# Kernel optimization log

Hardware: AMD Instinct MI355X
Metric: run time of the kernel (lower is better)

The kernel has to match this reference:

```python
import jax, jax.numpy as jnp
import numpy as np

KC = 32      # cluster_num
KS = 3       # kernel_size
AREA = KS * KS
ITERS = 10   # KMeans Lloyd iterations (fixed, deterministic init)


def _unfold3(x):
    # torch nn.Unfold(kernel_size=3, padding=1): feature dim ordered cin-major, area-minor
    b, c, h, w = x.shape
    xp = jnp.pad(x, ((0, 0), (0, 0), (1, 1), (1, 1)))
    cols = jnp.stack([xp[:, :, i:i + h, j:j + w] for i in range(KS) for j in range(KS)], axis=2)  # [b,c,area,h,w]
    return cols.reshape(b, c * AREA, h * w).transpose(0, 2, 1)  # [b, hw, c*area]


def _kmeans_assign(feat):
    # Lloyd's KMeans on [s, d] features; deterministic strided init; returns [s] int assignments
    s, d = feat.shape
    c0 = feat[jnp.arange(KC) * (s // KC)]
    f2 = (feat * feat).sum(-1, keepdims=True)
    def dists(c):
        return f2 - 2.0 * feat @ c.T + (c * c).sum(-1)[None, :]
    def step(c, _):
        idx = jnp.argmin(dists(c), axis=1)
        cnt = jax.ops.segment_sum(jnp.ones((s,), feat.dtype), idx, KC)
        sm = jax.ops.segment_sum(feat, idx, KC)
        c_new = jnp.where(cnt[:, None] > 0, sm / jnp.maximum(cnt, 1.0)[:, None], c)
        return c_new, None
    c, _ = jax.lax.scan(step, c0, None, length=ITERS)
    return jnp.argmin(dists(c), axis=1)


def _seg_mean(p, idx):
    # per-cluster mean of patches -> patch-space centroids [K, f]
    s = p.shape[0]
    cnt = jax.ops.segment_sum(jnp.ones((s,), p.dtype), idx, KC)
    return jax.ops.segment_sum(p, idx, KC) / jnp.maximum(cnt, 1.0)[:, None]


def _mlp2(x, W1, b1, W2, b2):
    return jax.nn.relu(jax.nn.relu(x @ W1 + b1) @ W2 + b2)


def setup_inputs():
    key = jax.random.key(0)
    ks = jax.random.split(key, 16)
    cin, cout, m = 32, 32, 16
    f = cin * AREA
    g = lambda k, shp, sc: jax.random.normal(k, shp, dtype=jnp.float32) * sc
    return {
        "x": g(ks[0], (4, cin, 64, 64), 1.0),
        "Wh1": g(ks[1], (f, m), (2.0 / f) ** 0.5), "bh1": jnp.zeros((m,), jnp.float32),
        "Wh2": g(ks[2], (m, m), (2.0 / m) ** 0.5), "bh2": jnp.zeros((m,), jnp.float32),
        "Wa": g(ks[3], (m, AREA), (2.0 / m) ** 0.5), "ba": jnp.zeros((AREA,), jnp.float32),
        "Wc": g(ks[4], (m, cin), (2.0 / m) ** 0.5), "bc": jnp.zeros((cin,), jnp.float32),
        "Wo": g(ks[5], (m, cout), (2.0 / m) ** 0.5), "bo": jnp.zeros((cout,), jnp.float32),
        "kernels": g(ks[6], (cin, AREA, cout), (2.0 / (cin * AREA)) ** 0.5),
        "Wb1": g(ks[7], (f, m), (2.0 / f) ** 0.5), "bb1": jnp.zeros((m,), jnp.float32),
        "Wb2": g(ks[8], (m, m), (2.0 / m) ** 0.5), "bb2": jnp.zeros((m,), jnp.float32),
        "Wb3": g(ks[9], (m, cout), (2.0 / m) ** 0.5), "bb3": jnp.zeros((cout,), jnp.float32),
    }


def reference(x, Wh1, bh1, Wh2, bh2, Wa, ba, Wc, bc, Wo, bo, kernels, Wb1, bb1, Wb2, bb2, Wb3, bb3):
    b, cin, h, w = x.shape
    s = h * w
    cout = kernels.shape[-1]
    patches = _unfold3(x)                                        # [b, s, cin*area]
    feat = patches.reshape(b, s, cin, AREA).mean(-1)             # cluster_source='channel'
    idx = jax.vmap(_kmeans_assign)(jax.lax.stop_gradient(feat))  # [b, s] cluster assignments
    centroids = jax.vmap(_seg_mean)(patches, idx)                # [b, K, cin*area]
    # low_rank kernel generator: rank-1 modulation along cin/area/cout of shared base kernel
    kf = _mlp2(centroids, Wh1, bh1, Wh2, bh2)                    # [b, K, m]
    w_cin = jax.nn.sigmoid(kf @ Wc + bc)                         # [b, K, cin]
    w_area = jax.nn.sigmoid(kf @ Wa + ba)                        # [b, K, area]
    w_cout = jax.nn.sigmoid(kf @ Wo + bo)                        # [b, K, cout]
    kern = (w_cin[:, :, :, None, None] * w_area[:, :, None, :, None]
            * w_cout[:, :, None, None, :] * kernels[None, None])  # [b, K, cin, area, cout]
    kern = kern.reshape(b, KC, cin * AREA, cout)
    bias = _mlp2(centroids, Wb1, bb1, Wb2, bb2) @ Wb3 + bb3      # [b, K, cout] (bias='cluster')
    # gather per-pixel kernel/bias by cluster id, grouped matmul, scatter back (dense-gather form)
    bi = jnp.arange(b)[:, None]
    Wpix = kern[bi, idx]                                         # [b, s, f, cout]
    out = jnp.einsum('bsf,bsfo->bso', patches, Wpix) + bias[bi, idx]
    return out.reshape(b, h, w, cout).transpose(0, 3, 1, 2), idx
```

## Files before the change

kernel.cpp:

```cpp
#include <hip/hip_runtime.h>
#include <stdint.h>

typedef unsigned long long u64;

#define Bn 4
#define CINn 32
#define Hn 64
#define Wn 64
#define Sn 4096
#define KCn 32
#define Mn 16
#define COUTn 32
#define AREAn 9
#define Fn 288
#define NITER 10
#define FXSCALE 4294967296.0
#define NBLK_B 32
#define LDK 292

#define AT_LD_U32(p)    __hip_atomic_load((p),  __ATOMIC_RELAXED, __HIP_MEMORY_SCOPE_AGENT)
#define AT_LD_U64(p)    __hip_atomic_load((p),  __ATOMIC_RELAXED, __HIP_MEMORY_SCOPE_AGENT)
#define AT_ST_U32(p,v)  __hip_atomic_store((p), (v), __ATOMIC_RELAXED, __HIP_MEMORY_SCOPE_AGENT)
#define AT_ST_U64(p,v)  __hip_atomic_store((p), (v), __ATOMIC_RELAXED, __HIP_MEMORY_SCOPE_AGENT)

static __device__ __forceinline__ float relu_(float v){ return v > 0.f ? v : 0.f; }
static __device__ __forceinline__ float sigmoid_(float v){ return 1.f / (1.f + expf(-v)); }

static __device__ __forceinline__ void batch_barrier(unsigned* bar){
    __syncthreads();
    if (threadIdx.x == 0){
        asm volatile("s_waitcnt vmcnt(0)" ::: "memory");
        unsigned* cnt = bar;
        unsigned* gen = bar + 32;
        unsigned g = __hip_atomic_load(gen, __ATOMIC_RELAXED, __HIP_MEMORY_SCOPE_AGENT);
        unsigned a = __hip_atomic_fetch_add(cnt, 1u, __ATOMIC_RELAXED, __HIP_MEMORY_SCOPE_AGENT);
        if (a == (unsigned)(NBLK_B - 1)){
            __hip_atomic_store(cnt, 0u, __ATOMIC_RELAXED, __HIP_MEMORY_SCOPE_AGENT);
            __hip_atomic_fetch_add(gen, 1u, __ATOMIC_RELAXED, __HIP_MEMORY_SCOPE_AGENT);
        } else {
            while (__hip_atomic_load(gen, __ATOMIC_RELAXED, __HIP_MEMORY_SCOPE_AGENT) == g)
                __builtin_amdgcn_s_sleep(4);
        }
    }
    __syncthreads();
}

__global__ __launch_bounds__(256) void k_init(const float* __restrict__ x,
                                              float* __restrict__ feat,
                                              u64* __restrict__ gsum,
                                              unsigned* __restrict__ gcnt,
                                              unsigned* __restrict__ bar){
    int g = blockIdx.x * 256 + threadIdx.x;
    if (g < 3 * Bn * KCn * CINn) gsum[g] = 0ull;
    if (g < 3 * Bn * KCn)        gcnt[g] = 0u;
    if (g < 4 * 64)              bar[g]  = 0u;
    int p = g & (Sn - 1);
    int c = (g >> 12) & (CINn - 1);
    int b = g >> 17;
    int y = p >> 6, xx = p & 63;
    const float* xc = x + ((size_t)(b * CINn + c) << 12);
    float s = 0.f;
    #pragma unroll
    for (int i = 0; i < 3; ++i){
        int yy = y + i - 1;
        if (yy < 0 || yy >= Hn) continue;
        #pragma unroll
        for (int j = 0; j < 3; ++j){
            int xj = xx + j - 1;
            if (xj < 0 || xj >= Wn) continue;
            s += xc[(yy << 6) + xj];
        }
    }
    feat[g] = s * (1.f / 9.f);
}

struct AssignSh {
    u64   fxL[128][32];
    u64   lsum[KCn][CINn];
    float cent[KCn][CINn];
    float c2[KCn];
    float bestd[256];
    int   bestk[256];
    int   bi128[128];
    unsigned lcnt[KCn];
    unsigned cntPrev[KCn];
    int   rankF[128];
    unsigned totK[KCn];
    unsigned goffK[KCn + 1];
    unsigned baseBT[KCn];
};
struct SmkSh {
    float psum[KCn][AREAn][8];
    float centL[Fn];
    int   pl[256];
    float part1[16][16], part2[16][16];
    float hL[2][Mn];
    float kfL[2][Mn];
};
union ShU { AssignSh a; SmkSh m; };

__global__ __launch_bounds__(256) void k_main(const float* __restrict__ x,
        const float* __restrict__ feat,
        u64* __restrict__ gsum, unsigned* __restrict__ gcnt,
        unsigned* __restrict__ blkcnt,
        int* __restrict__ idx, float* __restrict__ idxf,
        int* __restrict__ sorted,
        const float* __restrict__ Wh1, const float* __restrict__ bh1,
        const float* __restrict__ Wh2, const float* __restrict__ bh2,
        const float* __restrict__ Wa,  const float* __restrict__ ba,
        const float* __restrict__ Wc,  const float* __restrict__ bc,
        const float* __restrict__ Wo,  const float* __restrict__ bo,
        const float* __restrict__ Wb1, const float* __restrict__ bb1,
        const float* __restrict__ Wb2, const float* __restrict__ bb2,
        const float* __restrict__ Wb3, const float* __restrict__ bb3,
        float* __restrict__ wcin, float* __restrict__ warea,
        float* __restrict__ wcout, float* __restrict__ biasb,
        unsigned* __restrict__ bars){
    __shared__ ShU sh;
    const int tid  = threadIdx.x;
    const int b    = blockIdx.x >> 5;
    const int tnum = blockIdx.x & 31;
    unsigned* bar  = bars + b * 64;

    const int pxi  = tid & 127;
    const int half = tid >> 7;
    const int p    = tnum * 128 + pxi;

    float fv[CINn];
    #pragma unroll
    for (int c = 0; c < CINn; ++c) fv[c] = feat[(b * CINn + c) * Sn + p];
    float f2 = 0.f;
    #pragma unroll
    for (int c = 0; c < CINn; ++c) f2 = fmaf(fv[c], fv[c], f2);
    if (tid < 128){
        #pragma unroll
        for (int c = 0; c < CINn; ++c)
            sh.a.fxL[tid][c] = (u64)llrint((double)fv[c] * FXSCALE);
    }

    for (int iter = 0; iter <= NITER; ++iter){
        const int prev = (iter + 2) % 3;
        const int cur  = iter % 3;
        const int nxt  = (iter + 1) % 3;

        if (iter > 0 && tid < KCn)
            sh.a.cntPrev[tid] = AT_LD_U32(&gcnt[(prev * Bn + b) * KCn + tid]);
        __syncthreads();

        for (int e = tid; e < KCn * CINn; e += 256){
            int k = e >> 5, c = e & 31;
            if (iter == 0){
                sh.a.cent[k][c] = feat[(b * CINn + c) * Sn + k * (Sn / KCn)];
            } else {
                unsigned cn = sh.a.cntPrev[k];
                if (cn > 0){
                    u64 sv = AT_LD_U64(&gsum[((prev * Bn + b) * KCn + k) * CINn + c]);
                    sh.a.cent[k][c] = (float)((double)(long long)sv / ((double)cn * FXSCALE));
                }
            }
            sh.a.lsum[k][c] = 0ull;
            if (tnum == 0)
                AT_ST_U64(&gsum[((nxt * Bn + b) * KCn + k) * CINn + c], 0ull);
        }
        if (tnum == 0 && tid < KCn)
            AT_ST_U32(&gcnt[(nxt * Bn + b) * KCn + tid], 0u);
        __syncthreads();

        if (tid < 32){
            float s = 0.f;
            #pragma unroll
            for (int c = 0; c < CINn; ++c) s = fmaf(sh.a.cent[tid][c], sh.a.cent[tid][c], s);
            sh.a.c2[tid] = s;
        } else if (tid < 64){
            sh.a.lcnt[tid - 32] = 0u;
        }
        __syncthreads();

        float best = 3.402823466e38f;
        int   bk   = half << 4;
        #pragma unroll 4
        for (int k = 0; k < 16; ++k){
            const int kk = (half << 4) + k;
            const float4* cr4 = reinterpret_cast<const float4*>(sh.a.cent[kk]);
            float dot = 0.f;
            #pragma unroll
            for (int cq = 0; cq < 8; ++cq){
                float4 cv = cr4[cq];
                dot = fmaf(fv[cq * 4 + 0], cv.x, dot);
                dot = fmaf(fv[cq * 4 + 1], cv.y, dot);
                dot = fmaf(fv[cq * 4 + 2], cv.z, dot);
                dot = fmaf(fv[cq * 4 + 3], cv.w, dot);
            }
            float d = f2 - 2.f * dot + sh.a.c2[kk];
            if (d < best){ best = d; bk = kk; }
        }
        sh.a.bestd[tid] = best;
        sh.a.bestk[tid] = bk;
        __syncthreads();

        if (tid < 128){
            float d0 = sh.a.bestd[tid], d1 = sh.a.bestd[tid + 128];
            int   k0 = sh.a.bestk[tid], k1 = sh.a.bestk[tid + 128];
            int bi = (d1 < d0) ? k1 : k0;
            sh.a.bi128[tid] = bi;
            if (iter < NITER) atomicAdd(&sh.a.lcnt[bi], 1u);
        }
        __syncthreads();

        if (iter < NITER){
            {
                const int myk = sh.a.bi128[pxi];
                const int c0  = half << 4;
                #pragma unroll
                for (int c = 0; c < 16; ++c)
                    atomicAdd(&sh.a.lsum[myk][c0 + c], sh.a.fxL[pxi][c0 + c]);
            }
            __syncthreads();
            for (int e = tid; e < KCn * CINn; e += 256){
                int k = e >> 5, c = e & 31;
                u64 v = sh.a.lsum[k][c];
                if (v) atomicAdd(&gsum[((cur * Bn + b) * KCn + k) * CINn + c], v);
            }
            if (tid < KCn){
                unsigned v = sh.a.lcnt[tid];
                if (v) atomicAdd(&gcnt[(cur * Bn + b) * KCn + tid], v);
            }
        } else {
            if (tid < 128){
                int bi = sh.a.bi128[tid];
                idx [b * Sn + p] = bi;
                idxf[b * Sn + p] = (float)bi;
            }
            __syncthreads();
            if (tid < KCn){
                int r = 0;
                for (int q = 0; q < 128; ++q)
                    if (sh.a.bi128[q] == tid) sh.a.rankF[q] = r++;
                AT_ST_U32(&blkcnt[(b * KCn + tid) * NBLK_B + tnum], (unsigned)r);
            }
        }
        batch_barrier(bar);
    }

    if (tid < KCn){
        unsigned run = 0, mybase = 0;
        #pragma unroll 4
        for (int t2 = 0; t2 < NBLK_B; ++t2){
            unsigned v = AT_LD_U32(&blkcnt[(b * KCn + tid) * NBLK_B + t2]);
            if (t2 == tnum) mybase = run;
            run += v;
        }
        sh.a.totK[tid]   = run;
        sh.a.baseBT[tid] = mybase;
    }
    __syncthreads();
    if (tid == 0){
        unsigned acc = 0;
        #pragma unroll
        for (int k = 0; k < KCn; ++k){ sh.a.goffK[k] = acc; acc += sh.a.totK[k]; }
        sh.a.goffK[KCn] = acc;
    }
    __syncthreads();
    if (tid < 128){
        int k = sh.a.bi128[tid];
        unsigned pos = sh.a.goffK[k] + sh.a.baseBT[k] + (unsigned)sh.a.rankF[tid];
        AT_ST_U32((unsigned*)&sorted[b * Sn + pos], (unsigned)(tnum * 128 + tid));
    }
    const int kk    = tnum;
    const int off0r = (int)sh.a.goffK[kk];
    const int nmy   = (int)sh.a.totK[kk];
    batch_barrier(bar);

    {
        const int cA = tid >> 3;
        const int s  = tid & 7;
        const float* xc = x + ((size_t)(b * CINn + cA) << 12);
        float acc[9];
        #pragma unroll
        for (int a = 0; a < 9; ++a) acc[a] = 0.f;

        for (int base = 0; base < nmy; base += 256){
            int m = min(256, nmy - base);
            __syncthreads();
            if (tid < m)
                sh.m.pl[tid] = (int)AT_LD_U32((unsigned*)&sorted[b * Sn + off0r + base + tid]);
            __syncthreads();
            #pragma unroll 2
            for (int i = s; i < m; i += 8){
                int pp = sh.m.pl[i];
                int py = pp >> 6, px2 = pp & 63;
                #pragma unroll
                for (int a = 0; a < 9; ++a){
                    int y1 = py + a / 3 - 1, x1 = px2 + (a % 3) - 1;
                    float v = (y1 >= 0 && y1 < Hn && x1 >= 0 && x1 < Wn)
                              ? xc[(y1 << 6) + x1] : 0.f;
                    acc[a] += v;
                }
            }
        }
        __syncthreads();
        #pragma unroll
        for (int a = 0; a < 9; ++a) sh.m.psum[cA][a][s] = acc[a];
        __syncthreads();
        float invn = 1.f / (float)max(nmy, 1);
        for (int f = tid; f < Fn; f += 256){
            int c = f / 9, a = f - c * 9;
            float sm = 0.f;
            #pragma unroll
            for (int s2 = 0; s2 < 8; ++s2) sm += sh.m.psum[c][a][s2];
            sh.m.centL[f] = sm * invn;
        }
    }
    __syncthreads();

    {
        int j = tid & 15, rep = tid >> 4;
        float p1 = 0.f, p2 = 0.f;
        int fbeg = rep * 18;
        for (int ff = fbeg; ff < fbeg + 18; ++ff){
            float cv = sh.m.centL[ff];
            p1 = fmaf(cv, Wh1[ff * Mn + j], p1);
            p2 = fmaf(cv, Wb1[ff * Mn + j], p2);
        }
        sh.m.part1[rep][j] = p1;
        sh.m.part2[rep][j] = p2;
    }
    __syncthreads();
    if (tid < 32){
        int br = tid >> 4, j = tid & 15;
        float s = br ? bb1[j] : bh1[j];
        for (int r = 0; r < 16; ++r) s += br ? sh.m.part2[r][j] : sh.m.part1[r][j];
        sh.m.hL[br][j] = relu_(s);
    }
    __syncthreads();
    if (tid < 32){
        int br = tid >> 4, j = tid & 15;
        const float* W2 = br ? Wb2 : Wh2;
        float s = br ? bb2[j] : bh2[j];
        #pragma unroll
        for (int i = 0; i < Mn; ++i) s = fmaf(sh.m.hL[br][i], W2[i * Mn + j], s);
        sh.m.kfL[br][j] = relu_(s);
    }
    __syncthreads();
    if (tid < 32){
        int o = tid;
        float s1 = bc[o], s2 = bo[o], s3 = bb3[o];
        #pragma unroll
        for (int i = 0; i < Mn; ++i){
            float kv = sh.m.kfL[0][i];
            s1 = fmaf(kv, Wc[i * COUTn + o], s1);
            s2 = fmaf(kv, Wo[i * COUTn + o], s2);
            s3 = fmaf(sh.m.kfL[1][i], Wb3[i * COUTn + o], s3);
        }
        wcin [(b * KCn + kk) * CINn  + o] = sigmoid_(s1);
        wcout[(b * KCn + kk) * COUTn + o] = sigmoid_(s2);
        biasb[(b * KCn + kk) * COUTn + o] = s3;
    } else if (tid < 41){
        int a2 = tid - 32;
        float s = ba[a2];
        #pragma unroll
        for (int i = 0; i < Mn; ++i) s = fmaf(sh.m.kfL[0][i], Wa[i * AREAn + a2], s);
        warea[(b * KCn + kk) * AREAn + a2] = sigmoid_(s);
    }
}

__global__ __launch_bounds__(256) void k_out(const float* __restrict__ x,
                                             const int* __restrict__ sorted,
                                             const int* __restrict__ idx,
                                             const float* __restrict__ wcin,
                                             const float* __restrict__ warea,
                                             const float* __restrict__ wcout,
                                             const float* __restrict__ biasb,
                                             const float* __restrict__ kern0,
                                             float* __restrict__ out){
    int b    = blockIdx.x >> 7;
    int tile = blockIdx.x & 127;
    int tid  = threadIdx.x;

    __shared__ float kernT[KCn * LDK];
    __shared__ float patchL[32 * LDK];
    __shared__ int   pix[32];
    __shared__ int   kid[32];
    __shared__ float wcl[CINn], wal[AREAn], wol[COUTn], biasL[COUTn];

    if (tid < 32){
        int pp = sorted[b * Sn + tile * 32 + tid];
        pix[tid] = pp;
        kid[tid] = idx[b * Sn + pp];
    }
    int fA = tid;       int cA = fA / 9, aA = fA - cA * 9;
    int dyA = aA / 3 - 1, dxA = aA % 3 - 1;
    int fB = 256 + tid; int cB = fB / 9, aB = fB - cB * 9;
    int dyB = aB / 3 - 1, dxB = aB % 3 - 1;
    __syncthreads();

    #pragma unroll 4
    for (int px = 0; px < 32; ++px){
        int pp = pix[px];
        int py = pp >> 6, pxx = pp & 63;
        int y1 = py + dyA, x1 = pxx + dxA;
        patchL[px * LDK + tid] = (y1 >= 0 && y1 < Hn && x1 >= 0 && x1 < Wn)
            ? x[((size_t)(b * CINn + cA) << 12) + (y1 << 6) + x1] : 0.f;
        if (tid < 32){
            int y2 = py + dyB, x2 = pxx + dxB;
            patchL[px * LDK + 256 + tid] = (y2 >= 0 && y2 < Hn && x2 >= 0 && x2 < Wn)
                ? x[((size_t)(b * CINn + cB) << 12) + (y2 << 6) + x2] : 0.f;
        }
    }

    int o2 = tid & 15, p2 = tid >> 4;
    int oA = o2 * 2, oB = o2 * 2 + 1;
    int pxA = p2 * 2, pxB = p2 * 2 + 1;

    int i0 = 0;
    while (i0 < 32){
        __syncthreads();
        int kcur = kid[i0];
        int i1 = i0 + 1;
        while (i1 < 32 && kid[i1] == kcur) ++i1;

        if (tid < 32)       wcl[tid]        = wcin [(b * KCn + kcur) * CINn  + tid];
        else if (tid < 64)  wol[tid - 32]   = wcout[(b * KCn + kcur) * COUTn + tid - 32];
        else if (tid < 73)  wal[tid - 64]   = warea[(b * KCn + kcur) * AREAn + tid - 64];
        else if (tid >= 96 && tid < 128) biasL[tid - 96] = biasb[(b * KCn + kcur) * COUTn + tid - 96];
        __syncthreads();

        {
            int o  = tid >> 3;
            int q  = tid & 7;
            int f0 = q * 36;
            int cc = q * 4, aa = 0;
            float wo_ = wol[o];
            float* kr = kernT + o * LDK + f0;
            #pragma unroll 4
            for (int i2 = 0; i2 < 36; ++i2){
                kr[i2] = wcl[cc] * wal[aa] * wo_ * kern0[(f0 + i2) * COUTn + o];
                if (++aa == 9){ aa = 0; ++cc; }
            }
        }
        __syncthreads();

        bool actA = (pxA >= i0 && pxA < i1);
        bool actB = (pxB >= i0 && pxB < i1);
        if (actA || actB){
            const float* krA = kernT + oA * LDK;
            const float* krB = kernT + oB * LDK;
            const float* prA = patchL + pxA * LDK;
            const float* prB = patchL + pxB * LDK;
            float s00 = 0.f, s01 = 0.f, s10 = 0.f, s11 = 0.f;
            if (actA && actB){
                #pragma unroll 4
                for (int fq = 0; fq < Fn; fq += 4){
                    float4 k0 = *reinterpret_cast<const float4*>(krA + fq);
                    float4 k1 = *reinterpret_cast<const float4*>(krB + fq);
                    float4 pa = *reinterpret_cast<const float4*>(prA + fq);
                    float4 pb = *reinterpret_cast<const float4*>(prB + fq);
                    s00 = fmaf(pa.x,k0.x,s00); s00 = fmaf(pa.y,k0.y,s00); s00 = fmaf(pa.z,k0.z,s00); s00 = fmaf(pa.w,k0.w,s00);
                    s01 = fmaf(pa.x,k1.x,s01); s01 = fmaf(pa.y,k1.y,s01); s01 = fmaf(pa.z,k1.z,s01); s01 = fmaf(pa.w,k1.w,s01);
                    s10 = fmaf(pb.x,k0.x,s10); s10 = fmaf(pb.y,k0.y,s10); s10 = fmaf(pb.z,k0.z,s10); s10 = fmaf(pb.w,k0.w,s10);
                    s11 = fmaf(pb.x,k1.x,s11); s11 = fmaf(pb.y,k1.y,s11); s11 = fmaf(pb.z,k1.z,s11); s11 = fmaf(pb.w,k1.w,s11);
                }
            } else {
                const float* pr = actA ? prA : prB;
                #pragma unroll 4
                for (int fq = 0; fq < Fn; fq += 4){
                    float4 k0 = *reinterpret_cast<const float4*>(krA + fq);
                    float4 k1 = *reinterpret_cast<const float4*>(krB + fq);
                    float4 pa = *reinterpret_cast<const float4*>(pr + fq);
                    s00 = fmaf(pa.x,k0.x,s00); s00 = fmaf(pa.y,k0.y,s00); s00 = fmaf(pa.z,k0.z,s00); s00 = fmaf(pa.w,k0.w,s00);
                    s01 = fmaf(pa.x,k1.x,s01); s01 = fmaf(pa.y,k1.y,s01); s01 = fmaf(pa.z,k1.z,s01); s01 = fmaf(pa.w,k1.w,s01);
                }
                if (actB){ s10 = s00; s11 = s01; s00 = 0.f; s01 = 0.f; }
            }
            if (actA){
                int pp = pix[pxA];
                out[((size_t)(b * COUTn + oA) << 12) + pp] = biasL[oA] + s00;
                out[((size_t)(b * COUTn + oB) << 12) + pp] = biasL[oB] + s01;
            }
            if (actB){
                int pp = pix[pxB];
                out[((size_t)(b * COUTn + oA) << 12) + pp] = biasL[oA] + s10;
                out[((size_t)(b * COUTn + oB) << 12) + pp] = biasL[oB] + s11;
            }
        }
        i0 = i1;
    }
}

extern "C" void kernel_launch(void* const* d_in, const int* in_sizes, int n_in,
                              void* d_out, int out_size, void* d_ws, size_t ws_size,
                              hipStream_t stream){
    const float* x    = (const float*)d_in[0];
    const float* Wh1  = (const float*)d_in[1];
    const float* bh1  = (const float*)d_in[2];
    const float* Wh2  = (const float*)d_in[3];
    const float* bh2  = (const float*)d_in[4];
    const float* Wa   = (const float*)d_in[5];
    const float* ba   = (const float*)d_in[6];
    const float* Wc   = (const float*)d_in[7];
    const float* bc   = (const float*)d_in[8];
    const float* Wo   = (const float*)d_in[9];
    const float* bo   = (const float*)d_in[10];
    const float* kern0= (const float*)d_in[11];
    const float* Wb1  = (const float*)d_in[12];
    const float* bb1  = (const float*)d_in[13];
    const float* Wb2  = (const float*)d_in[14];
    const float* bb2  = (const float*)d_in[15];
    const float* Wb3  = (const float*)d_in[16];
    const float* bb3  = (const float*)d_in[17];

    char* ws = (char*)d_ws;
    float*    feat   = (float*)(ws + 0);
    u64*      gsum   = (u64*)  (ws + 2097152);
    unsigned* gcnt   = (unsigned*)(ws + 2195456);
    unsigned* blkcnt = (unsigned*)(ws + 2196992);
    int*      idx    = (int*)  (ws + 2213376);
    int*      sorted = (int*)  (ws + 2278912);
    float*    wcin   = (float*)(ws + 2344448);
    float*    warea  = (float*)(ws + 2360832);
    float*    wcout  = (float*)(ws + 2365440);
    float*    biasb  = (float*)(ws + 2381824);
    unsigned* bars   = (unsigned*)(ws + 2398208);

    float* outp = (float*)d_out;
    float* idxf = outp + (size_t)Bn * COUTn * Sn;

    k_init<<<(Bn * CINn * Sn) / 256, 256, 0, stream>>>(x, feat, gsum, gcnt, bars);
    k_main<<<Bn * NBLK_B, 256, 0, stream>>>(x, feat, gsum, gcnt, blkcnt, idx, idxf,
                                            sorted,
                                            Wh1, bh1, Wh2, bh2, Wa, ba, Wc, bc, Wo, bo,
                                            Wb1, bb1, Wb2, bb2, Wb3, bb3,
                                            wcin, warea, wcout, biasb, bars);
    k_out<<<Bn * 128, 256, 0, stream>>>(x, sorted, idx, wcin, warea, wcout, biasb,
                                        kern0, outp);
}
```

Baseline: 225.5 us.

## Restructure k-means reduction, patch centroid accumulation and output chunking per cluster

Halves the blocks per batch to 16 with one pixel per thread. Each block now writes its own partial sums and counts, and every block reduces over all block partials, so global atomics and the triple-buffered zeroing go away. Patch-space centroids are accumulated per block in shared memory and atomically added to a global buffer, so each cluster no longer gathers its own pixels after the barrier. The output kernel launches one block per 32-pixel chunk of a single cluster using a precomputed chunk map, which removes the in-block loop over mixed clusters. The risks are fewer blocks for the k-means phase and heavier shared-memory float atomics.

```diff
diff --git a/kernel.cpp b/kernel.cpp
--- a/kernel.cpp
+++ b/kernel.cpp
@@ -15,11 +15,14 @@
 #define Fn 288
 #define NITER 10
 #define FXSCALE 4294967296.0
-#define NBLK_B 32
+#define NBLK_B 16
+#define PXB 256
+#define CMAX 160
 #define LDK 292
 
 #define AT_LD_U32(p)    __hip_atomic_load((p),  __ATOMIC_RELAXED, __HIP_MEMORY_SCOPE_AGENT)
 #define AT_LD_U64(p)    __hip_atomic_load((p),  __ATOMIC_RELAXED, __HIP_MEMORY_SCOPE_AGENT)
+#define AT_LD_F32(p)    __hip_atomic_load((p),  __ATOMIC_RELAXED, __HIP_MEMORY_SCOPE_AGENT)
 #define AT_ST_U32(p,v)  __hip_atomic_store((p), (v), __ATOMIC_RELAXED, __HIP_MEMORY_SCOPE_AGENT)
 #define AT_ST_U64(p,v)  __hip_atomic_store((p), (v), __ATOMIC_RELAXED, __HIP_MEMORY_SCOPE_AGENT)
 
@@ -39,7 +42,7 @@
             __hip_atomic_fetch_add(gen, 1u, __ATOMIC_RELAXED, __HIP_MEMORY_SCOPE_AGENT);
         } else {
             while (__hip_atomic_load(gen, __ATOMIC_RELAXED, __HIP_MEMORY_SCOPE_AGENT) == g)
-                __builtin_amdgcn_s_sleep(4);
+                __builtin_amdgcn_s_sleep(2);
         }
     }
     __syncthreads();
@@ -47,13 +50,11 @@
 
 __global__ __launch_bounds__(256) void k_init(const float* __restrict__ x,
                                               float* __restrict__ feat,
-                                              u64* __restrict__ gsum,
-                                              unsigned* __restrict__ gcnt,
+                                              float* __restrict__ gpsum,
                                               unsigned* __restrict__ bar){
     int g = blockIdx.x * 256 + threadIdx.x;
-    if (g < 3 * Bn * KCn * CINn) gsum[g] = 0ull;
-    if (g < 3 * Bn * KCn)        gcnt[g] = 0u;
-    if (g < 4 * 64)              bar[g]  = 0u;
+    if (g < Bn * KCn * Fn) gpsum[g] = 0.f;
+    if (g < Bn * 64)       bar[g]   = 0u;
     int p = g & (Sn - 1);
     int c = (g >> 12) & (CINn - 1);
     int b = g >> 17;
@@ -75,24 +76,17 @@
 }
 
 struct AssignSh {
-    u64   fxL[128][32];
-    u64   lsum[KCn][CINn];
     float cent[KCn][CINn];
     float c2[KCn];
-    float bestd[256];
-    int   bestk[256];
-    int   bi128[128];
+    u64   lsum[KCn][CINn];
     unsigned lcnt[KCn];
-    unsigned cntPrev[KCn];
-    int   rankF[128];
-    unsigned totK[KCn];
-    unsigned goffK[KCn + 1];
+    unsigned cntTot[KCn];
+    int   rankF[PXB];
     unsigned baseBT[KCn];
 };
 struct SmkSh {
-    float psum[KCn][AREAn][8];
+    float psum[KCn][Fn];
     float centL[Fn];
-    int   pl[256];
     float part1[16][16], part2[16][16];
     float hL[2][Mn];
     float kfL[2][Mn];
@@ -101,10 +95,10 @@
 
 __global__ __launch_bounds__(256) void k_main(const float* __restrict__ x,
         const float* __restrict__ feat,
-        u64* __restrict__ gsum, unsigned* __restrict__ gcnt,
+        u64* __restrict__ bsum, unsigned* __restrict__ bcnt,
         unsigned* __restrict__ blkcnt,
         int* __restrict__ idx, float* __restrict__ idxf,
-        int* __restrict__ sorted,
+        int* __restrict__ sorted, int4* __restrict__ chunk_map,
         const float* __restrict__ Wh1, const float* __restrict__ bh1,
         const float* __restrict__ Wh2, const float* __restrict__ bh2,
         const float* __restrict__ Wa,  const float* __restrict__ ba,
@@ -115,16 +109,18 @@
         const float* __restrict__ Wb3, const float* __restrict__ bb3,
         float* __restrict__ wcin, float* __restrict__ warea,
         float* __restrict__ wcout, float* __restrict__ biasb,
+        float* __restrict__ gpsum,
         unsigned* __restrict__ bars){
+    __shared__ int bi256[PXB];
+    __shared__ unsigned totK[KCn];
+    __shared__ unsigned goffK[KCn + 1];
     __shared__ ShU sh;
+
     const int tid  = threadIdx.x;
-    const int b    = blockIdx.x >> 5;
-    const int tnum = blockIdx.x & 31;
+    const int b    = blockIdx.x >> 4;
+    const int tnum = blockIdx.x & 15;
     unsigned* bar  = bars + b * 64;
-
-    const int pxi  = tid & 127;
-    const int half = tid >> 7;
-    const int p    = tnum * 128 + pxi;
+    const int p    = tnum * PXB + tid;
 
     float fv[CINn];
     #pragma unroll
@@ -132,56 +128,49 @@
     float f2 = 0.f;
     #pragma unroll
     for (int c = 0; c < CINn; ++c) f2 = fmaf(fv[c], fv[c], f2);
-    if (tid < 128){
-        #pragma unroll
-        for (int c = 0; c < CINn; ++c)
-            sh.a.fxL[tid][c] = (u64)llrint((double)fv[c] * FXSCALE);
-    }
 
     for (int iter = 0; iter <= NITER; ++iter){
-        const int prev = (iter + 2) % 3;
-        const int cur  = iter % 3;
-        const int nxt  = (iter + 1) % 3;
-
-        if (iter > 0 && tid < KCn)
-            sh.a.cntPrev[tid] = AT_LD_U32(&gcnt[(prev * Bn + b) * KCn + tid]);
-        __syncthreads();
-
-        for (int e = tid; e < KCn * CINn; e += 256){
-            int k = e >> 5, c = e & 31;
-            if (iter == 0){
+        if (iter == 0){
+            for (int e = tid; e < KCn * CINn; e += 256){
+                int k = e >> 5, c = e & 31;
                 sh.a.cent[k][c] = feat[(b * CINn + c) * Sn + k * (Sn / KCn)];
-            } else {
-                unsigned cn = sh.a.cntPrev[k];
-                if (cn > 0){
-                    u64 sv = AT_LD_U64(&gsum[((prev * Bn + b) * KCn + k) * CINn + c]);
-                    sh.a.cent[k][c] = (float)((double)(long long)sv / ((double)cn * FXSCALE));
-                }
-            }
-            sh.a.lsum[k][c] = 0ull;
-            if (tnum == 0)
-                AT_ST_U64(&gsum[((nxt * Bn + b) * KCn + k) * CINn + c], 0ull);
-        }
-        if (tnum == 0 && tid < KCn)
-            AT_ST_U32(&gcnt[(nxt * Bn + b) * KCn + tid], 0u);
-        __syncthreads();
-
-        if (tid < 32){
+            }
+        } else {
+            if (tid < KCn){
+                unsigned s = 0;
+                #pragma unroll 4
+                for (int blk = 0; blk < NBLK_B; ++blk)
+                    s += AT_LD_U32(&bcnt[(b * NBLK_B + blk) * KCn + tid]);
+                sh.a.cntTot[tid] = s;
+            }
+            __syncthreads();
+            for (int e = tid; e < KCn * CINn; e += 256){
+                int k = e >> 5, c = e & 31;
+                u64 s = 0;
+                #pragma unroll 4
+                for (int blk = 0; blk < NBLK_B; ++blk)
+                    s += AT_LD_U64(&bsum[((size_t)(b * NBLK_B + blk) * KCn + k) * CINn + c]);
+                unsigned cn = sh.a.cntTot[k];
+                if (cn > 0)
+                    sh.a.cent[k][c] = (float)((double)(long long)s / ((double)cn * FXSCALE));
+            }
+        }
+        __syncthreads();
+        if (tid < KCn){
             float s = 0.f;
             #pragma unroll
             for (int c = 0; c < CINn; ++c) s = fmaf(sh.a.cent[tid][c], sh.a.cent[tid][c], s);
             sh.a.c2[tid] = s;
-        } else if (tid < 64){
-            sh.a.lcnt[tid - 32] = 0u;
-        }
-        __syncthreads();
-
-        float best = 3.402823466e38f;
-        int   bk   = half << 4;
+            sh.a.lcnt[tid] = 0u;
+        }
+        for (int e = tid; e < KCn * CINn; e += 256)
+            ((u64*)sh.a.lsum)[e] = 0ull;
+        __syncthreads();
+
+        float best = 3.402823466e38f; int bk = 0;
         #pragma unroll 4
-        for (int k = 0; k < 16; ++k){
-            const int kk = (half << 4) + k;
-            const float4* cr4 = reinterpret_cast<const float4*>(sh.a.cent[kk]);
+        for (int k = 0; k < KCn; ++k){
+            const float4* cr4 = reinterpret_cast<const float4*>(sh.a.cent[k]);
             float dot = 0.f;
             #pragma unroll
             for (int cq = 0; cq < 8; ++cq){
@@ -191,51 +180,34 @@
                 dot = fmaf(fv[cq * 4 + 2], cv.z, dot);
                 dot = fmaf(fv[cq * 4 + 3], cv.w, dot);
             }
-            float d = f2 - 2.f * dot + sh.a.c2[kk];
-            if (d < best){ best = d; bk = kk; }
-        }
-        sh.a.bestd[tid] = best;
-        sh.a.bestk[tid] = bk;
-        __syncthreads();
-
-        if (tid < 128){
-            float d0 = sh.a.bestd[tid], d1 = sh.a.bestd[tid + 128];
-            int   k0 = sh.a.bestk[tid], k1 = sh.a.bestk[tid + 128];
-            int bi = (d1 < d0) ? k1 : k0;
-            sh.a.bi128[tid] = bi;
-            if (iter < NITER) atomicAdd(&sh.a.lcnt[bi], 1u);
-        }
-        __syncthreads();
+            float d = f2 - 2.f * dot + sh.a.c2[k];
+            if (d < best){ best = d; bk = k; }
+        }
+        bi256[tid] = bk;
 
         if (iter < NITER){
-            {
-                const int myk = sh.a.bi128[pxi];
-                const int c0  = half << 4;
-                #pragma unroll
-                for (int c = 0; c < 16; ++c)
-                    atomicAdd(&sh.a.lsum[myk][c0 + c], sh.a.fxL[pxi][c0 + c]);
+            atomicAdd(&sh.a.lcnt[bk], 1u);
+            #pragma unroll
+            for (int c = 0; c < CINn; ++c){
+                u64 q = (u64)llrint((double)fv[c] * FXSCALE);
+                atomicAdd(&sh.a.lsum[bk][c], q);
             }
             __syncthreads();
             for (int e = tid; e < KCn * CINn; e += 256){
                 int k = e >> 5, c = e & 31;
-                u64 v = sh.a.lsum[k][c];
-                if (v) atomicAdd(&gsum[((cur * Bn + b) * KCn + k) * CINn + c], v);
-            }
-            if (tid < KCn){
-                unsigned v = sh.a.lcnt[tid];
-                if (v) atomicAdd(&gcnt[(cur * Bn + b) * KCn + tid], v);
-            }
+                AT_ST_U64(&bsum[((size_t)(b * NBLK_B + tnum) * KCn + k) * CINn + c],
+                          sh.a.lsum[k][c]);
+            }
+            if (tid < KCn)
+                AT_ST_U32(&bcnt[(b * NBLK_B + tnum) * KCn + tid], sh.a.lcnt[tid]);
         } else {
-            if (tid < 128){
-                int bi = sh.a.bi128[tid];
-                idx [b * Sn + p] = bi;
-                idxf[b * Sn + p] = (float)bi;
-            }
+            idx [b * Sn + p] = bk;
+            idxf[b * Sn + p] = (float)bk;
             __syncthreads();
             if (tid < KCn){
                 int r = 0;
-                for (int q = 0; q < 128; ++q)
-                    if (sh.a.bi128[q] == tid) sh.a.rankF[q] = r++;
+                for (int q = 0; q < PXB; ++q)
+                    if (bi256[q] == tid) sh.a.rankF[q] = r++;
                 AT_ST_U32(&blkcnt[(b * KCn + tid) * NBLK_B + tnum], (unsigned)r);
             }
         }
@@ -245,245 +217,228 @@
     if (tid < KCn){
         unsigned run = 0, mybase = 0;
         #pragma unroll 4
-        for (int t2 = 0; t2 < NBLK_B; ++t2){
-            unsigned v = AT_LD_U32(&blkcnt[(b * KCn + tid) * NBLK_B + t2]);
-            if (t2 == tnum) mybase = run;
+        for (int blk = 0; blk < NBLK_B; ++blk){
+            unsigned v = AT_LD_U32(&blkcnt[(b * KCn + tid) * NBLK_B + blk]);
+            if (blk == tnum) mybase = run;
             run += v;
         }
-        sh.a.totK[tid]   = run;
+        totK[tid] = run;
         sh.a.baseBT[tid] = mybase;
     }
     __syncthreads();
     if (tid == 0){
         unsigned acc = 0;
         #pragma unroll
-        for (int k = 0; k < KCn; ++k){ sh.a.goffK[k] = acc; acc += sh.a.totK[k]; }
-        sh.a.goffK[KCn] = acc;
-    }
-    __syncthreads();
-    if (tid < 128){
-        int k = sh.a.bi128[tid];
-        unsigned pos = sh.a.goffK[k] + sh.a.baseBT[k] + (unsigned)sh.a.rankF[tid];
-        AT_ST_U32((unsigned*)&sorted[b * Sn + pos], (unsigned)(tnum * 128 + tid));
-    }
-    const int kk    = tnum;
-    const int off0r = (int)sh.a.goffK[kk];
-    const int nmy   = (int)sh.a.totK[kk];
+        for (int k = 0; k < KCn; ++k){ goffK[k] = acc; acc += totK[k]; }
+        goffK[KCn] = acc;
+    }
+    __syncthreads();
+    {
+        int k = bi256[tid];
+        unsigned pos = goffK[k] + sh.a.baseBT[k] + (unsigned)sh.a.rankF[tid];
+        sorted[b * Sn + pos] = p;
+    }
+    if (tnum == 0 && tid == 0){
+        int j = 0;
+        for (int k = 0; k < KCn; ++k){
+            int n = (int)totK[k];
+            for (int cb = 0; cb < n; cb += 32){
+                chunk_map[b * CMAX + j] = make_int4(k, (int)goffK[k] + cb, min(32, n - cb), 0);
+                ++j;
+            }
+        }
+        for (; j < CMAX; ++j) chunk_map[b * CMAX + j] = make_int4(-1, 0, 0, 0);
+    }
+    __syncthreads();
+
+    for (int e = tid; e < KCn * Fn; e += 256) ((float*)sh.m.psum)[e] = 0.f;
+    __syncthreads();
+    {
+        const int cc   = tid >> 3;
+        const int slot = tid & 7;
+        const float* xc = x + ((size_t)(b * CINn + cc) << 12);
+        for (int i = slot; i < PXB; i += 8){
+            int k  = bi256[i];
+            int pp = tnum * PXB + i;
+            int py = pp >> 6, px2 = pp & 63;
+            float* ps = &sh.m.psum[k][cc * 9];
+            #pragma unroll
+            for (int a = 0; a < 9; ++a){
+                int y1 = py + a / 3 - 1, x1 = px2 + (a % 3) - 1;
+                float v = (y1 >= 0 && y1 < Hn && x1 >= 0 && x1 < Wn)
+                          ? xc[(y1 << 6) + x1] : 0.f;
+                atomicAdd(&ps[a], v);
+            }
+        }
+    }
+    __syncthreads();
+    for (int e = tid; e < KCn * Fn; e += 256){
+        float v = ((float*)sh.m.psum)[e];
+        if (v != 0.f) atomicAdd(&gpsum[(size_t)b * KCn * Fn + e], v);
+    }
     batch_barrier(bar);
 
-    {
-        const int cA = tid >> 3;
-        const int s  = tid & 7;
-        const float* xc = x + ((size_t)(b * CINn + cA) << 12);
-        float acc[9];
-        #pragma unroll
-        for (int a = 0; a < 9; ++a) acc[a] = 0.f;
-
-        for (int base = 0; base < nmy; base += 256){
-            int m = min(256, nmy - base);
-            __syncthreads();
-            if (tid < m)
-                sh.m.pl[tid] = (int)AT_LD_U32((unsigned*)&sorted[b * Sn + off0r + base + tid]);
-            __syncthreads();
-            #pragma unroll 2
-            for (int i = s; i < m; i += 8){
-                int pp = sh.m.pl[i];
-                int py = pp >> 6, px2 = pp & 63;
-                #pragma unroll
-                for (int a = 0; a < 9; ++a){
-                    int y1 = py + a / 3 - 1, x1 = px2 + (a % 3) - 1;
-                    float v = (y1 >= 0 && y1 < Hn && x1 >= 0 && x1 < Wn)
-                              ? xc[(y1 << 6) + x1] : 0.f;
-                    acc[a] += v;
-                }
-            }
-        }
-        __syncthreads();
-        #pragma unroll
-        for (int a = 0; a < 9; ++a) sh.m.psum[cA][a][s] = acc[a];
-        __syncthreads();
-        float invn = 1.f / (float)max(nmy, 1);
-        for (int f = tid; f < Fn; f += 256){
-            int c = f / 9, a = f - c * 9;
-            float sm = 0.f;
-            #pragma unroll
-            for (int s2 = 0; s2 < 8; ++s2) sm += sh.m.psum[c][a][s2];
-            sh.m.centL[f] = sm * invn;
-        }
-    }
-    __syncthreads();
-
-    {
-        int j = tid & 15, rep = tid >> 4;
-        float p1 = 0.f, p2 = 0.f;
-        int fbeg = rep * 18;
-        for (int ff = fbeg; ff < fbeg + 18; ++ff){
-            float cv = sh.m.centL[ff];
-            p1 = fmaf(cv, Wh1[ff * Mn + j], p1);
-            p2 = fmaf(cv, Wb1[ff * Mn + j], p2);
-        }
-        sh.m.part1[rep][j] = p1;
-        sh.m.part2[rep][j] = p2;
-    }
-    __syncthreads();
-    if (tid < 32){
-        int br = tid >> 4, j = tid & 15;
-        float s = br ? bb1[j] : bh1[j];
-        for (int r = 0; r < 16; ++r) s += br ? sh.m.part2[r][j] : sh.m.part1[r][j];
-        sh.m.hL[br][j] = relu_(s);
-    }
-    __syncthreads();
-    if (tid < 32){
-        int br = tid >> 4, j = tid & 15;
-        const float* W2 = br ? Wb2 : Wh2;
-        float s = br ? bb2[j] : bh2[j];
-        #pragma unroll
-        for (int i = 0; i < Mn; ++i) s = fmaf(sh.m.hL[br][i], W2[i * Mn + j], s);
-        sh.m.kfL[br][j] = relu_(s);
-    }
-    __syncthreads();
-    if (tid < 32){
-        int o = tid;
-        float s1 = bc[o], s2 = bo[o], s3 = bb3[o];
-        #pragma unroll
-        for (int i = 0; i < Mn; ++i){
-            float kv = sh.m.kfL[0][i];
-            s1 = fmaf(kv, Wc[i * COUTn + o], s1);
-            s2 = fmaf(kv, Wo[i * COUTn + o], s2);
-            s3 = fmaf(sh.m.kfL[1][i], Wb3[i * COUTn + o], s3);
-        }
-        wcin [(b * KCn + kk) * CINn  + o] = sigmoid_(s1);
-        wcout[(b * KCn + kk) * COUTn + o] = sigmoid_(s2);
-        biasb[(b * KCn + kk) * COUTn + o] = s3;
-    } else if (tid < 41){
-        int a2 = tid - 32;
-        float s = ba[a2];
-        #pragma unroll
-        for (int i = 0; i < Mn; ++i) s = fmaf(sh.m.kfL[0][i], Wa[i * AREAn + a2], s);
-        warea[(b * KCn + kk) * AREAn + a2] = sigmoid_(s);
+    for (int kq = 0; kq < 2; ++kq){
+        const int kk = tnum + kq * 16;
+        const float invn = 1.f / (float)max(totK[kk], 1u);
+        __syncthreads();
+        for (int f = tid; f < Fn; f += 256)
+            sh.m.centL[f] = AT_LD_F32(&gpsum[((size_t)b * KCn + kk) * Fn + f]) * invn;
+        __syncthreads();
+        {
+            int j = tid & 15, rep = tid >> 4;
+            float p1 = 0.f, p2 = 0.f;
+            int fbeg = rep * 18;
+            for (int ff = fbeg; ff < fbeg + 18; ++ff){
+                float cv = sh.m.centL[ff];
+                p1 = fmaf(cv, Wh1[ff * Mn + j], p1);
+                p2 = fmaf(cv, Wb1[ff * Mn + j], p2);
+            }
+            sh.m.part1[rep][j] = p1;
+            sh.m.part2[rep][j] = p2;
+        }
+        __syncthreads();
+        if (tid < 32){
+            int br = tid >> 4, j = tid & 15;
+            float s = br ? bb1[j] : bh1[j];
+            for (int r = 0; r < 16; ++r) s += br ? sh.m.part2[r][j] : sh.m.part1[r][j];
+            sh.m.hL[br][j] = relu_(s);
+        }
+        __syncthreads();
+        if (tid < 32){
+            int br = tid >> 4, j = tid & 15;
+            const float* W2 = br ? Wb2 : Wh2;
+            float s = br ? bb2[j] : bh2[j];
+            #pragma unroll
+            for (int i = 0; i < Mn; ++i) s = fmaf(sh.m.hL[br][i], W2[i * Mn + j], s);
+            sh.m.kfL[br][j] = relu_(s);
+        }
+        __syncthreads();
+        if (tid < 32){
+            int o = tid;
+            float s1 = bc[o], s2 = bo[o], s3 = bb3[o];
+            #pragma unroll
+            for (int i = 0; i < Mn; ++i){
+                float kv = sh.m.kfL[0][i];
+                s1 = fmaf(kv, Wc[i * COUTn + o], s1);
+                s2 = fmaf(kv, Wo[i * COUTn + o], s2);
+                s3 = fmaf(sh.m.kfL[1][i], Wb3[i * COUTn + o], s3);
+            }
+            wcin [(b * KCn + kk) * CINn  + o] = sigmoid_(s1);
+            wcout[(b * KCn + kk) * COUTn + o] = sigmoid_(s2);
+            biasb[(b * KCn + kk) * COUTn + o] = s3;
+        } else if (tid < 41){
+            int a2 = tid - 32;
+            float s = ba[a2];
+            #pragma unroll
+            for (int i = 0; i < Mn; ++i) s = fmaf(sh.m.kfL[0][i], Wa[i * AREAn + a2], s);
+            warea[(b * KCn + kk) * AREAn + a2] = sigmoid_(s);
+        }
     }
 }
 
 __global__ __launch_bounds__(256) void k_out(const float* __restrict__ x,
                                              const int* __restrict__ sorted,
-                                             const int* __restrict__ idx,
+                                             const int4* __restrict__ chunk_map,
                                              const float* __restrict__ wcin,
                                              const float* __restrict__ warea,
                                              const float* __restrict__ wcout,
                                              const float* __restrict__ biasb,
                                              const float* __restrict__ kern0,
                                              float* __restrict__ out){
-    int b    = blockIdx.x >> 7;
-    int tile = blockIdx.x & 127;
-    int tid  = threadIdx.x;
-
-    __shared__ float kernT[KCn * LDK];
+    const int b   = blockIdx.x / CMAX;
+    const int j   = blockIdx.x - b * CMAX;
+    const int tid = threadIdx.x;
+
+    int4 cm = chunk_map[b * CMAX + j];
+    const int kcur = cm.x;
+    if (kcur < 0) return;
+    const int base = cm.y;
+    const int cnt  = cm.z;
+
+    __shared__ float kernT[COUTn * LDK];
     __shared__ float patchL[32 * LDK];
     __shared__ int   pix[32];
-    __shared__ int   kid[32];
     __shared__ float wcl[CINn], wal[AREAn], wol[COUTn], biasL[COUTn];
 
     if (tid < 32){
-        int pp = sorted[b * Sn + tile * 32 + tid];
-        pix[tid] = pp;
-        kid[tid] = idx[b * Sn + pp];
-    }
-    int fA = tid;       int cA = fA / 9, aA = fA - cA * 9;
-    int dyA = aA / 3 - 1, dxA = aA % 3 - 1;
-    int fB = 256 + tid; int cB = fB / 9, aB = fB - cB * 9;
-    int dyB = aB / 3 - 1, dxB = aB % 3 - 1;
-    __syncthreads();
+        pix[tid] = (tid < cnt) ? sorted[b * Sn + base + tid] : -1;
+    } else if (tid < 64)  wcl[tid - 32]    = wcin [(b * KCn + kcur) * CINn  + tid - 32];
+    else if (tid < 96)    wol[tid - 64]    = wcout[(b * KCn + kcur) * COUTn + tid - 64];
+    else if (tid < 105)   wal[tid - 96]    = warea[(b * KCn + kcur) * AREAn + tid - 96];
+    else if (tid >= 128 && tid < 160) biasL[tid - 128] = biasb[(b * KCn + kcur) * COUTn + tid - 128];
+
+    const int fA = tid;       const int cA = fA / 9, aA = fA - cA * 9;
+    const int dyA = aA / 3 - 1, dxA = aA % 3 - 1;
+    const int fB = 256 + tid; const int cB = fB / 9, aB = fB - cB * 9;
+    const int dyB = aB / 3 - 1, dxB = aB % 3 - 1;
+    __syncthreads();
+
+    {
+        int o  = tid >> 3;
+        int q  = tid & 7;
+        int f0 = q * 36;
+        int cc = q * 4, aa = 0;
+        float wo_ = wol[o];
+        float* kr = kernT + o * LDK + f0;
+        #pragma unroll 4
+        for (int i2 = 0; i2 < 36; ++i2){
+            kr[i2] = wcl[cc] * wal[aa] * wo_ * kern0[(f0 + i2) * COUTn + o];
+            if (++aa == 9){ aa = 0; ++cc; }
+        }
+    }
 
     #pragma unroll 4
     for (int px = 0; px < 32; ++px){
         int pp = pix[px];
-        int py = pp >> 6, pxx = pp & 63;
-        int y1 = py + dyA, x1 = pxx + dxA;
-        patchL[px * LDK + tid] = (y1 >= 0 && y1 < Hn && x1 >= 0 && x1 < Wn)
-            ? x[((size_t)(b * CINn + cA) << 12) + (y1 << 6) + x1] : 0.f;
-        if (tid < 32){
-            int y2 = py + dyB, x2 = pxx + dxB;
-            patchL[px * LDK + 256 + tid] = (y2 >= 0 && y2 < Hn && x2 >= 0 && x2 < Wn)
-                ? x[((size_t)(b * CINn + cB) << 12) + (y2 << 6) + x2] : 0.f;
-        }
-    }
-
-    int o2 = tid & 15, p2 = tid >> 4;
-    int oA = o2 * 2, oB = o2 * 2 + 1;
-    int pxA = p2 * 2, pxB = p2 * 2 + 1;
-
-    int i0 = 0;
-    while (i0 < 32){
-        __syncthreads();
-        int kcur = kid[i0];
-        int i1 = i0 + 1;
-        while (i1 < 32 && kid[i1] == kcur) ++i1;
-
-        if (tid < 32)       wcl[tid]        = wcin [(b * KCn + kcur) * CINn  + tid];
-        else if (tid < 64)  wol[tid - 32]   = wcout[(b * KCn + kcur) * COUTn + tid - 32];
-        else if (tid < 73)  wal[tid - 64]   = warea[(b * KCn + kcur) * AREAn + tid - 64];
-        else if (tid >= 96 && tid < 128) biasL[tid - 96] = biasb[(b * KCn + kcur) * COUTn + tid - 96];
-        __syncthreads();
-
-        {
-            int o  = tid >> 3;
-            int q  = tid & 7;
-            int f0 = q * 36;
-            int cc = q * 4, aa = 0;
-            float wo_ = wol[o];
-            float* kr = kernT + o * LDK + f0;
-            #pragma unroll 4
-            for (int i2 = 0; i2 < 36; ++i2){
-                kr[i2] = wcl[cc] * wal[aa] * wo_ * kern0[(f0 + i2) * COUTn + o];
-                if (++aa == 9){ aa = 0; ++cc; }
-            }
-        }
-        __syncthreads();
-
-        bool actA = (pxA >= i0 && pxA < i1);
-        bool actB = (pxB >= i0 && pxB < i1);
-        if (actA || actB){
-            const float* krA = kernT + oA * LDK;
-            const float* krB = kernT + oB * LDK;
-            const float* prA = patchL + pxA * LDK;
-            const float* prB = patchL + pxB * LDK;
-            float s00 = 0.f, s01 = 0.f, s10 = 0.f, s11 = 0.f;
-            if (actA && actB){
-                #pragma unroll 4
-                for (int fq = 0; fq < Fn; fq += 4){
-                    float4 k0 = *reinterpret_cast<const float4*>(krA + fq);
-                    float4 k1 = *reinterpret_cast<const float4*>(krB + fq);
-                    float4 pa = *reinterpret_cast<const float4*>(prA + fq);
-                    float4 pb = *reinterpret_cast<const float4*>(prB + fq);
-                    s00 = fmaf(pa.x,k0.x,s00); s00 = fmaf(pa.y,k0.y,s00); s00 = fmaf(pa.z,k0.z,s00); s00 = fmaf(pa.w,k0.w,s00);
-                    s01 = fmaf(pa.x,k1.x,s01); s01 = fmaf(pa.y,k1.y,s01); s01 = fmaf(pa.z,k1.z,s01); s01 = fmaf(pa.w,k1.w,s01);
-                    s10 = fmaf(pb.x,k0.x,s10); s10 = fmaf(pb.y,k0.y,s10); s10 = fmaf(pb.z,k0.z,s10); s10 = fmaf(pb.w,k0.w,s10);
-                    s11 = fmaf(pb.x,k1.x,s11); s11 = fmaf(pb.y,k1.y,s11); s11 = fmaf(pb.z,k1.z,s11); s11 = fmaf(pb.w,k1.w,s11);
-                }
-            } else {
-                const float* pr = actA ? prA : prB;
-                #pragma unroll 4
-                for (int fq = 0; fq < Fn; fq += 4){
-                    float4 k0 = *reinterpret_cast<const float4*>(krA + fq);
-                    float4 k1 = *reinterpret_cast<const float4*>(krB + fq);
-                    float4 pa = *reinterpret_cast<const float4*>(pr + fq);
-                    s00 = fmaf(pa.x,k0.x,s00); s00 = fmaf(pa.y,k0.y,s00); s00 = fmaf(pa.z,k0.z,s00); s00 = fmaf(pa.w,k0.w,s00);
-                    s01 = fmaf(pa.x,k1.x,s01); s01 = fmaf(pa.y,k1.y,s01); s01 = fmaf(pa.z,k1.z,s01); s01 = fmaf(pa.w,k1.w,s01);
-                }
-                if (actB){ s10 = s00; s11 = s01; s00 = 0.f; s01 = 0.f; }
-            }
-            if (actA){
-                int pp = pix[pxA];
-                out[((size_t)(b * COUTn + oA) << 12) + pp] = biasL[oA] + s00;
-                out[((size_t)(b * COUTn + oB) << 12) + pp] = biasL[oB] + s01;
-            }
-            if (actB){
-                int pp = pix[pxB];
-                out[((size_t)(b * COUTn + oA) << 12) + pp] = biasL[oA] + s10;
-                out[((size_t)(b * COUTn + oB) << 12) + pp] = biasL[oB] + s11;
-            }
-        }
-        i0 = i1;
+        float vA = 0.f, vB = 0.f;
+        if (pp >= 0){
+            int py = pp >> 6, pxx = pp & 63;
+            int y1 = py + dyA, x1 = pxx + dxA;
+            if (y1 >= 0 && y1 < Hn && x1 >= 0 && x1 < Wn)
+                vA = x[((size_t)(b * CINn + cA) << 12) + (y1 << 6) + x1];
+            if (tid < 32){
+                int y2 = py + dyB, x2 = pxx + dxB;
+                if (y2 >= 0 && y2 < Hn && x2 >= 0 && x2 < Wn)
+                    vB = x[((size_t)(b * CINn + cB) << 12) + (y2 << 6) + x2];
+            }
+        }
+        patchL[px * LDK + tid] = vA;
+        if (tid < 32) patchL[px * LDK + 256 + tid] = vB;
+    }
+    __syncthreads();
+
+    const int o2 = tid & 15, p2 = tid >> 4;
+    const int oA = o2 * 2, oB = o2 * 2 + 1;
+    const int pxA = p2 * 2, pxB = p2 * 2 + 1;
+    const bool actA = pxA < cnt, actB = pxB < cnt;
+    if (!actA && !actB) return;
+
+    const float* krA = kernT + oA * LDK;
+    const float* krB = kernT + oB * LDK;
+    const float* prA = patchL + pxA * LDK;
+    const float* prB = patchL + pxB * LDK;
+    float s00 = 0.f, s01 = 0.f, s10 = 0.f, s11 = 0.f;
+    #pragma unroll 4
+    for (int fq = 0; fq < Fn; fq += 4){
+        float4 k0 = *reinterpret_cast<const float4*>(krA + fq);
+        float4 k1 = *reinterpret_cast<const float4*>(krB + fq);
+        float4 pa = *reinterpret_cast<const float4*>(prA + fq);
+        float4 pb = *reinterpret_cast<const float4*>(prB + fq);
+        s00 = fmaf(pa.x,k0.x,s00); s00 = fmaf(pa.y,k0.y,s00); s00 = fmaf(pa.z,k0.z,s00); s00 = fmaf(pa.w,k0.w,s00);
+        s01 = fmaf(pa.x,k1.x,s01); s01 = fmaf(pa.y,k1.y,s01); s01 = fmaf(pa.z,k1.z,s01); s01 = fmaf(pa.w,k1.w,s01);
+        s10 = fmaf(pb.x,k0.x,s10); s10 = fmaf(pb.y,k0.y,s10); s10 = fmaf(pb.z,k0.z,s10); s10 = fmaf(pb.w,k0.w,s10);
+        s11 = fmaf(pb.x,k1.x,s11); s11 = fmaf(pb.y,k1.y,s11); s11 = fmaf(pb.z,k1.z,s11); s11 = fmaf(pb.w,k1.w,s11);
+    }
+    if (actA){
+        int pp = pix[pxA];
+        out[((size_t)(b * COUTn + oA) << 12) + pp] = biasL[oA] + s00;
+        out[((size_t)(b * COUTn + oB) << 12) + pp] = biasL[oB] + s01;
+    }
+    if (actB){
+        int pp = pix[pxB];
+        out[((size_t)(b * COUTn + oA) << 12) + pp] = biasL[oA] + s10;
+        out[((size_t)(b * COUTn + oB) << 12) + pp] = biasL[oB] + s11;
     }
 }
 
@@ -511,26 +466,28 @@
 
     char* ws = (char*)d_ws;
     float*    feat   = (float*)(ws + 0);
-    u64*      gsum   = (u64*)  (ws + 2097152);
-    unsigned* gcnt   = (unsigned*)(ws + 2195456);
-    unsigned* blkcnt = (unsigned*)(ws + 2196992);
-    int*      idx    = (int*)  (ws + 2213376);
-    int*      sorted = (int*)  (ws + 2278912);
-    float*    wcin   = (float*)(ws + 2344448);
-    float*    warea  = (float*)(ws + 2360832);
-    float*    wcout  = (float*)(ws + 2365440);
-    float*    biasb  = (float*)(ws + 2381824);
-    unsigned* bars   = (unsigned*)(ws + 2398208);
+    u64*      bsum   = (u64*)  (ws + 2097152);
+    unsigned* bcnt   = (unsigned*)(ws + 2621440);
+    unsigned* blkcnt = (unsigned*)(ws + 2629632);
+    int*      idx    = (int*)  (ws + 2637824);
+    int*      sorted = (int*)  (ws + 2703360);
+    float*    gpsum  = (float*)(ws + 2768896);
+    float*    wcin   = (float*)(ws + 2916352);
+    float*    warea  = (float*)(ws + 2932736);
+    float*    wcout  = (float*)(ws + 2937344);
+    float*    biasb  = (float*)(ws + 2953728);
+    int4*     chunk_map = (int4*)(ws + 2970112);
+    unsigned* bars   = (unsigned*)(ws + 2980352);
 
     float* outp = (float*)d_out;
     float* idxf = outp + (size_t)Bn * COUTn * Sn;
 
-    k_init<<<(Bn * CINn * Sn) / 256, 256, 0, stream>>>(x, feat, gsum, gcnt, bars);
-    k_main<<<Bn * NBLK_B, 256, 0, stream>>>(x, feat, gsum, gcnt, blkcnt, idx, idxf,
-                                            sorted,
+    k_init<<<(Bn * CINn * Sn) / 256, 256, 0, stream>>>(x, feat, gpsum, bars);
+    k_main<<<Bn * NBLK_B, 256, 0, stream>>>(x, feat, bsum, bcnt, blkcnt, idx, idxf,
+                                            sorted, chunk_map,
                                             Wh1, bh1, Wh2, bh2, Wa, ba, Wc, bc, Wo, bo,
                                             Wb1, bb1, Wb2, bb2, Wb3, bb3,
-                                            wcin, warea, wcout, biasb, bars);
-    k_out<<<Bn * 128, 256, 0, stream>>>(x, sorted, idx, wcin, warea, wcout, biasb,
-                                        kern0, outp);
+                                            wcin, warea, wcout, biasb, gpsum, bars);
+    k_out<<<Bn * CMAX, 256, 0, stream>>>(x, sorted, chunk_map, wcin, warea, wcout,
+                                         biasb, kern0, outp);
 }
```

Result: slower. 445.8 us (+97.7%).
